# Optimization experiments

Measured on AMD Instinct MI355X. Metric: run time of the kernel, lower is better.

Reference implementation:

```python
import jax, jax.numpy as jnp
import numpy as np

N_CHAINS, L, Q, M, T_ROUNDS = 16384, 48, 4, 4, 7
BETA = 1.0


def setup_inputs() -> dict:
    key = jax.random.key(0)
    k1, k2, k3, k4 = jax.random.split(key, 4)
    # chains are one-hot encoded sequences [N, L, Q]
    cats = jax.random.randint(k1, (N_CHAINS, L), 0, Q)
    chains = jax.nn.one_hot(cats, Q, dtype=jnp.float32)
    h0 = jax.random.normal(k2, (L, Q), jnp.float32) * 0.1          # round-zero fields
    modes_h = jax.random.normal(k3, (M, L, Q), jnp.float32) * 0.1  # per-mode fields
    sel = jax.random.bernoulli(k4, 0.5, (T_ROUNDS, M))
    sel = sel.at[:, 0].set(True)  # ensure each round selects >=1 mode (avoid all -inf logsumexp)
    return {"chains": chains, "h0": h0, "modes_h": modes_h,
            "selected_modes": sel, "t": 7, "n_sweeps": 1}


def _selection_energy(x, modes_h, selected):
    # MultiModeDistribution.compute_energy
    # per-mode field energies: E_m(x) = -sum_{l} h_m[l] . x[l]  -> [N, M]
    en = -jnp.einsum('nlq,mlq->nm', x, modes_h)
    # normalized=True branch
    en = en - jax.nn.logsumexp(en, axis=1, keepdims=True)
    log_sel = jnp.log(selected.astype(x.dtype))                # [R, M], -inf where not selected
    # -( (-en[:,None,:] + log_sel).logsumexp(-1) ).sum(-1)
    per_round = jax.nn.logsumexp(-en[:, None, :] + log_sel[None, :, :], axis=-1)  # [N, R]
    return -jnp.sum(per_round, axis=-1)


def _energy_up_to_round(x, h0, modes_h, selected_modes, t):
    # compute_energy_up_to_round; t is a static Python int
    if t == -1:
        return jnp.zeros(x.shape[0], dtype=x.dtype)
    logNs0 = jnp.einsum('nlq,lq->n', x, h0)  # -round_zero.compute_energy(x), E0 = -h.x
    if t == 0:
        logps = jnp.zeros_like(logNs0)
    else:
        # linear-chain tree: ancestors_of(t-1) == [0, ..., t-1]
        logps = -_selection_energy(x, modes_h, selected_modes[:t])
    return -(logps + logNs0)


def reference(chains, h0, modes_h, selected_modes, t, n_sweeps):
    n_chains, L_, q = chains.shape
    n_steps = n_sweeps * L_
    energy = lambda x: _energy_up_to_round(x, h0, modes_h, selected_modes, t)

    def step(ch, k):
        k_idx, k_res, k_acc = jax.random.split(k, 3)
        idx = jax.random.randint(k_idx, (), 0, L_)                      # one site for all chains
        res_new = jax.nn.one_hot(jax.random.randint(k_res, (n_chains,), 0, q),
                                 q, dtype=ch.dtype)                     # [N, q]
        ch_new = ch.at[:, idx, :].set(res_new)
        delta_e = energy(ch_new) - energy(ch)                           # [N]
        rand_vals = jax.random.uniform(k_acc, (n_chains,), dtype=ch.dtype)
        accepted = jnp.exp(-BETA * delta_e) > rand_vals                 # [N]
        ch = jnp.where(accepted[:, None, None], ch_new, ch)
        return ch, None

    keys = jax.random.split(jax.random.key(42), n_steps)
    out, _ = jax.lax.scan(step, chains, keys)
    return out
```

## Files before the change

kernel.cpp:

```cpp
#include <hip/hip_runtime.h>
#include <math.h>


constexpr int kN = 16384;
constexpr int kL = 48;
constexpr int kM = 4;
constexpr int kR = 7;
constexpr int kSteps = 48;

#define TF_ROUND(rot) do { x0 += x1; x1 = (x1 << (rot)) | (x1 >> (32 - (rot))); x1 ^= x0; } while (0)

__device__ __forceinline__ void tf2(unsigned ka, unsigned kb,
                                    unsigned x0, unsigned x1,
                                    unsigned& o0, unsigned& o1) {
  const unsigned ks2 = ka ^ kb ^ 0x1BD11BDAu;
  x0 += ka; x1 += kb;
  TF_ROUND(13); TF_ROUND(15); TF_ROUND(26); TF_ROUND(6);
  x0 += kb; x1 += ks2 + 1u;
  TF_ROUND(17); TF_ROUND(29); TF_ROUND(16); TF_ROUND(24);
  x0 += ks2; x1 += ka + 2u;
  TF_ROUND(13); TF_ROUND(15); TF_ROUND(26); TF_ROUND(6);
  x0 += ka; x1 += kb + 3u;
  TF_ROUND(17); TF_ROUND(29); TF_ROUND(16); TF_ROUND(24);
  x0 += kb; x1 += ks2 + 4u;
  TF_ROUND(13); TF_ROUND(15); TF_ROUND(26); TF_ROUND(6);
  x0 += ks2; x1 += ka + 5u;
  o0 = x0; o1 = x1;
}

__device__ __forceinline__ unsigned rb32(unsigned ka, unsigned kb, unsigned i) {
  unsigned o0, o1; tf2(ka, kb, 0u, i, o0, o1); return o0 ^ o1;
}

__device__ __forceinline__ double pow7(double x) {
  const double x2 = x * x, x4 = x2 * x2;
  return x4 * x2 * x;
}

__device__ __forceinline__ unsigned catAt(unsigned w0, unsigned w1, unsigned w2,
                                          unsigned site) {
  const unsigned ww = (site < 16u) ? w0 : ((site < 32u) ? w1 : w2);
  return (ww >> (2u * (site & 15u))) & 3u;
}

#define PINV(x) asm volatile("" : "+v"(x))

__global__ __launch_bounds__(256)
void draw_kernel(unsigned* __restrict__ draws) {
  const unsigned s = blockIdx.y;
  const unsigned n = blockIdx.x * 256u + threadIdx.x;
  unsigned ka, kb;  tf2(0u, 42u, 0u, s, ka, kb);
  unsigned r0, r1, a0, a1, c0, c1;
  tf2(ka, kb, 0u, 1u, r0, r1);
  tf2(ka, kb, 0u, 2u, a0, a1);
  tf2(r0, r1, 0u, 1u, c0, c1);
  const unsigned nc = rb32(c0, c1, n) & 3u;
  const unsigned ub = rb32(a0, a1, n);
  draws[s * (unsigned)kN + n] = (ub & 0xFFFFFE00u) | nc;
}

__device__ __forceinline__ void build_selB(const void* selp, double (*sB)[4]) {
  const unsigned* wp = (const unsigned*)selp;
  int mode;
  if (wp[0] == 0x3F800000u) mode = 0;
  else {
    mode = 1;
    for (int i = 0; i < kR * kM; ++i) if (wp[i] > 1u) { mode = 2; break; }
  }
  for (int r = 0; r < kR; ++r)
    for (int m = 0; m < kM; ++m) {
      const int i = r * 4 + m;
      unsigned b;
      if (mode == 0)      b = (wp[i] == 0x3F800000u) ? 1u : 0u;
      else if (mode == 1) b = wp[i] ? 1u : 0u;
      else                b = ((const unsigned char*)selp)[i] ? 1u : 0u;
      sB[r][m] = b ? 1.0 : 0.0;
    }
}

__global__ __launch_bounds__(64, 1)
void mcmc_unrolled(const float* __restrict__ chains, const float* __restrict__ h0,
                   const float* __restrict__ modes_h, const void* __restrict__ selp,
                   const unsigned* __restrict__ draws, float* __restrict__ out) {
  __shared__ double2 sEH[kL][4];
  __shared__ double2 sEM[kM][kL][4];
  __shared__ double  sFH[kL][16];
  __shared__ double2 sFM[kM][kL][16];
  __shared__ unsigned sSite[64];
  __shared__ double sB[kR][4];

  const int tid = threadIdx.x;
  const int n = blockIdx.x * 64 + tid;

  for (int i = tid; i < kL * 4; i += 64) {
    const double v = (double)h0[i];
    sEH[i >> 2][i & 3] = make_double2(exp(v), exp(-v));
  }
  for (int i = tid; i < kM * kL * 4; i += 64) {
    const double v = (double)modes_h[i];
    sEM[i / (kL * 4)][(i >> 2) % kL][i & 3] = make_double2(exp(v), exp(-v));
  }

  {
    const unsigned s = (unsigned)tid;
    if (s < (unsigned)kSteps) {
      unsigned ka, kb;  tf2(0u, 42u, 0u, s, ka, kb);
      unsigned i0, i1, h1a, h1b, l1a, l1b;
      tf2(ka, kb, 0u, 0u, i0, i1);
      tf2(i0, i1, 0u, 0u, h1a, h1b);
      tf2(i0, i1, 0u, 1u, l1a, l1b);
      const unsigned hb = rb32(h1a, h1b, 0u);
      const unsigned lb = rb32(l1a, l1b, 0u);
      sSite[s] = ((hb % 48u) * 16u + (lb % 48u)) % 48u;
    } else {
      sSite[s] = 0u;
    }
  }
  if (tid == 0) build_selB(selp, sB);
  __syncthreads();

  for (int i = tid; i < kL * 16; i += 64) {
    const int l = i >> 4, p = i & 15, nw = p >> 2, od = p & 3;
    sFH[l][p] = sEH[l][nw].x * sEH[l][od].y;
#pragma unroll
    for (int m = 0; m < kM; ++m)
      sFM[m][l][p] = make_double2(sEM[m][l][nw].x * sEM[m][l][od].y,
                                  sEM[m][l][nw].y * sEM[m][l][od].x);
  }
  __syncthreads();

  unsigned dws[kSteps];
#pragma unroll
  for (int s = 0; s < kSteps; ++s) dws[s] = draws[(size_t)s * kN + n];

  unsigned w0 = 0, w1 = 0, w2 = 0;
  {
    const float4* ch = (const float4*)(chains + (size_t)n * (kL * 4));
#pragma unroll
    for (int l = 0; l < kL; ++l) {
      const float4 v = ch[l];
      const unsigned c = (v.y > 0.5f) ? 1u : ((v.z > 0.5f) ? 2u : ((v.w > 0.5f) ? 3u : 0u));
      const unsigned sh = 2u * (unsigned)(l & 15);
      if (l < 16) w0 |= c << sh; else if (l < 32) w1 |= c << sh; else w2 |= c << sh;
    }
  }

  double bb[kR][4];
#pragma unroll
  for (int r = 0; r < kR; ++r)
#pragma unroll
    for (int m = 0; m < 4; ++m) { bb[r][m] = sB[r][m]; PINV(bb[r][m]); }

  double e0 = 1.0, e1 = 1.0, e2 = 1.0, e3 = 1.0;
  double d0 = 1.0, d1 = 1.0, d2 = 1.0, d3 = 1.0;
#pragma unroll 4
  for (int l = 0; l < kL; ++l) {
    const unsigned c = catAt(w0, w1, w2, (unsigned)l);
    const double2 t0 = sEM[0][l][c], t1 = sEM[1][l][c];
    const double2 t2 = sEM[2][l][c], t3 = sEM[3][l][c];
    e0 *= t0.x; d0 *= t0.y;  e1 *= t1.x; d1 *= t1.y;
    e2 *= t2.x; d2 *= t2.y;  e3 *= t3.x; d3 *= t3.y;
  }
  double Dd = pow7((d0 + d1) + (d2 + d3));
#pragma unroll
  for (int r = 0; r < kR; ++r)
    Dd *= (fma(bb[r][1], e1, bb[r][0] * e0) + fma(bb[r][3], e3, bb[r][2] * e2));

#pragma unroll
  for (int s = 0; s < kSteps; ++s) PINV(dws[s]);

  unsigned site_c = sSite[0];
  unsigned nc_c = dws[0] & 3u;
  double fh_c;  double2 fm_c[4];
  {
    const unsigned idx = nc_c * 4u + catAt(w0, w1, w2, site_c);
    fh_c = sFH[site_c][idx];
#pragma unroll
    for (int m = 0; m < 4; ++m) fm_c[m] = sFM[m][site_c][idx];
  }

#pragma unroll
  for (int s = 0; s < kSteps; ++s) {
    const bool last = (s == kSteps - 1);

    unsigned site_n = 0, nc_n = 0, oldc_n = 0;
    double fh_n = 0.0;  double2 fm_n[4];
    if (!last) {
      site_n = sSite[s + 1];
      nc_n = dws[s + 1] & 3u;
      oldc_n = catAt(w0, w1, w2, site_n);
      const unsigned i1 = nc_n * 4u + oldc_n;
      fh_n = sFH[site_n][i1];
#pragma unroll
      for (int m = 0; m < 4; ++m) fm_n[m] = sFM[m][site_n][i1];
    }

    const float rndf = __uint_as_float((dws[s] >> 9) | 0x3F800000u) - 1.0f;
    const double f0 = e0 * fm_c[0].x, g0 = d0 * fm_c[0].y;
    const double f1 = e1 * fm_c[1].x, g1 = d1 * fm_c[1].y;
    const double f2 = e2 * fm_c[2].x, g2 = d2 * fm_c[2].y;
    const double f3 = e3 * fm_c[3].x, g3 = d3 * fm_c[3].y;
    double se[kR];
#pragma unroll
    for (int r = 0; r < kR; ++r)
      se[r] = fma(bb[r][1], f1, bb[r][0] * f0) + fma(bb[r][3], f3, bb[r][2] * f2);
    const double PQ = (pow7((g0 + g1) + (g2 + g3)) *
                       ((se[0] * se[1]) * (se[2] * se[3]))) *
                      ((se[4] * se[5]) * se[6]);
    const double N = fh_c * PQ;
    const bool acc = N > (double)rndf * Dd;

    const unsigned sh = 2u * (site_c & 15u);
    const unsigned mb = 3u << sh, nv = nc_c << sh;
    const bool in0 = site_c < 16u, in1 = (site_c >= 16u) & (site_c < 32u);
    w0 = (acc && in0) ? ((w0 & ~mb) | nv) : w0;
    w1 = (acc && in1) ? ((w1 & ~mb) | nv) : w1;
    w2 = (acc && !(in0 || in1)) ? ((w2 & ~mb) | nv) : w2;
    e0 = acc ? f0 : e0; e1 = acc ? f1 : e1; e2 = acc ? f2 : e2; e3 = acc ? f3 : e3;
    d0 = acc ? g0 : d0; d1 = acc ? g1 : d1; d2 = acc ? g2 : d2; d3 = acc ? g3 : d3;
    Dd = acc ? PQ : Dd;

    if (!last) {
      if (site_n == site_c) {
        const unsigned to = acc ? nc_c : oldc_n;
        const unsigned i2 = nc_n * 4u + to;
        fh_n = sFH[site_n][i2];
#pragma unroll
        for (int m = 0; m < 4; ++m) fm_n[m] = sFM[m][site_n][i2];
      }
      site_c = site_n; nc_c = nc_n;
      fh_c = fh_n;
#pragma unroll
      for (int m = 0; m < 4; ++m) fm_c[m] = fm_n[m];
    }
  }

  float4* o = (float4*)(out + (size_t)n * (kL * 4));
#pragma unroll
  for (int l = 0; l < kL; ++l) {
    const unsigned c = catAt(w0, w1, w2, (unsigned)l);
    o[l] = make_float4(c == 0u ? 1.0f : 0.0f, c == 1u ? 1.0f : 0.0f,
                       c == 2u ? 1.0f : 0.0f, c == 3u ? 1.0f : 0.0f);
  }
}

__global__ __launch_bounds__(64, 1)
void mcmc_loop(const float* __restrict__ chains, const float* __restrict__ h0,
               const float* __restrict__ modes_h, const void* __restrict__ selp,
               float* __restrict__ out) {
  __shared__ double2 sEH[kL][4];
  __shared__ double2 sEM[kM][kL][4];
  __shared__ double  sFH[kL][16];
  __shared__ double2 sFM[kM][kL][16];
  __shared__ unsigned sSite[64];
  __shared__ uint2 sCK[64], sAK[64];
  __shared__ double sB[kR][4];

  const int tid = threadIdx.x;
  for (int i = tid; i < kL * 4; i += 64) {
    const double v = (double)h0[i];
    sEH[i >> 2][i & 3] = make_double2(exp(v), exp(-v));
  }
  for (int i = tid; i < kM * kL * 4; i += 64) {
    const double v = (double)modes_h[i];
    sEM[i / (kL * 4)][(i >> 2) % kL][i & 3] = make_double2(exp(v), exp(-v));
  }
  {
    const unsigned s = (unsigned)tid;
    if (s < (unsigned)kSteps) {
      unsigned ka, kb;  tf2(0u, 42u, 0u, s, ka, kb);
      unsigned i0, i1, r0, r1, a0, a1;
      tf2(ka, kb, 0u, 0u, i0, i1);
      tf2(ka, kb, 0u, 1u, r0, r1);
      tf2(ka, kb, 0u, 2u, a0, a1);
      unsigned h1a, h1b, l1a, l1b;
      tf2(i0, i1, 0u, 0u, h1a, h1b);
      tf2(i0, i1, 0u, 1u, l1a, l1b);
      const unsigned hb = rb32(h1a, h1b, 0u);
      const unsigned lb = rb32(l1a, l1b, 0u);
      sSite[s] = ((hb % 48u) * 16u + (lb % 48u)) % 48u;
      unsigned c0, c1;  tf2(r0, r1, 0u, 1u, c0, c1);
      sCK[s] = make_uint2(c0, c1);
      sAK[s] = make_uint2(a0, a1);
    } else {
      sSite[s] = 0u; sCK[s] = make_uint2(0u, 0u); sAK[s] = make_uint2(0u, 0u);
    }
  }
  if (tid == 0) build_selB(selp, sB);
  __syncthreads();
  for (int i = tid; i < kL * 16; i += 64) {
    const int l = i >> 4, p = i & 15, nw = p >> 2, od = p & 3;
    sFH[l][p] = sEH[l][nw].x * sEH[l][od].y;
#pragma unroll
    for (int m = 0; m < kM; ++m)
      sFM[m][l][p] = make_double2(sEM[m][l][nw].x * sEM[m][l][od].y,
                                  sEM[m][l][nw].y * sEM[m][l][od].x);
  }
  __syncthreads();

  const int n = blockIdx.x * 64 + tid;
  double bb[kR][4];
#pragma unroll
  for (int r = 0; r < kR; ++r)
#pragma unroll
    for (int m = 0; m < 4; ++m) { bb[r][m] = sB[r][m]; PINV(bb[r][m]); }

  unsigned w0 = 0, w1 = 0, w2 = 0;
  {
    const float4* ch = (const float4*)(chains + (size_t)n * (kL * 4));
#pragma unroll
    for (int l = 0; l < kL; ++l) {
      const float4 v = ch[l];
      const unsigned c = (v.y > 0.5f) ? 1u : ((v.z > 0.5f) ? 2u : ((v.w > 0.5f) ? 3u : 0u));
      const unsigned sh = 2u * (unsigned)(l & 15);
      if (l < 16) w0 |= c << sh; else if (l < 32) w1 |= c << sh; else w2 |= c << sh;
    }
  }
  double e0 = 1.0, e1 = 1.0, e2 = 1.0, e3 = 1.0;
  double d0 = 1.0, d1 = 1.0, d2 = 1.0, d3 = 1.0;
#pragma unroll 4
  for (int l = 0; l < kL; ++l) {
    const unsigned c = catAt(w0, w1, w2, (unsigned)l);
    const double2 t0 = sEM[0][l][c], t1 = sEM[1][l][c];
    const double2 t2 = sEM[2][l][c], t3 = sEM[3][l][c];
    e0 *= t0.x; d0 *= t0.y;  e1 *= t1.x; d1 *= t1.y;
    e2 *= t2.x; d2 *= t2.y;  e3 *= t3.x; d3 *= t3.y;
  }
  double Dd = pow7((d0 + d1) + (d2 + d3));
#pragma unroll
  for (int r = 0; r < kR; ++r)
    Dd *= (fma(bb[r][1], e1, bb[r][0] * e0) + fma(bb[r][3], e3, bb[r][2] * e2));

  unsigned dw_c, dw_n;
  { const uint2 c0 = sCK[0], a0 = sAK[0];
    dw_c = (rb32(a0.x, a0.y, (unsigned)n) & 0xFFFFFE00u) |
           (rb32(c0.x, c0.y, (unsigned)n) & 3u); }
  { const uint2 c1 = sCK[1], a1 = sAK[1];
    dw_n = (rb32(a1.x, a1.y, (unsigned)n) & 0xFFFFFE00u) |
           (rb32(c1.x, c1.y, (unsigned)n) & 3u); }

  unsigned site_c = sSite[0];
  unsigned nc_c = dw_c & 3u;
  double fh_c;  double2 fm_c[4];
  {
    const unsigned idx = nc_c * 4u + catAt(w0, w1, w2, site_c);
    fh_c = sFH[site_c][idx];
#pragma unroll
    for (int m = 0; m < 4; ++m) fm_c[m] = sFM[m][site_c][idx];
  }

  for (int s = 0; s < kSteps; ++s) {
    const uint2 c2 = sCK[s + 2], a2 = sAK[s + 2];
    const unsigned dw_f = (rb32(a2.x, a2.y, (unsigned)n) & 0xFFFFFE00u) |
                          (rb32(c2.x, c2.y, (unsigned)n) & 3u);
    const unsigned site_n = sSite[s + 1];
    const unsigned nc_n = dw_n & 3u;
    const unsigned oldc_n = catAt(w0, w1, w2, site_n);
    double fh_n = sFH[site_n][nc_n * 4u + oldc_n];
    double2 fm_n[4];
#pragma unroll
    for (int m = 0; m < 4; ++m) fm_n[m] = sFM[m][site_n][nc_n * 4u + oldc_n];

    const float rndf = __uint_as_float((dw_c >> 9) | 0x3F800000u) - 1.0f;
    const double f0 = e0 * fm_c[0].x, g0 = d0 * fm_c[0].y;
    const double f1 = e1 * fm_c[1].x, g1 = d1 * fm_c[1].y;
    const double f2 = e2 * fm_c[2].x, g2 = d2 * fm_c[2].y;
    const double f3 = e3 * fm_c[3].x, g3 = d3 * fm_c[3].y;
    double se[kR];
#pragma unroll
    for (int r = 0; r < kR; ++r)
      se[r] = fma(bb[r][1], f1, bb[r][0] * f0) + fma(bb[r][3], f3, bb[r][2] * f2);
    const double PQ = (pow7((g0 + g1) + (g2 + g3)) *
                       ((se[0] * se[1]) * (se[2] * se[3]))) *
                      ((se[4] * se[5]) * se[6]);
    const double N = fh_c * PQ;
    const bool acc = N > (double)rndf * Dd;

    const unsigned sh = 2u * (site_c & 15u);
    const unsigned mb = 3u << sh, nv = nc_c << sh;
    const bool in0 = site_c < 16u, in1 = (site_c >= 16u) & (site_c < 32u);
    w0 = (acc && in0) ? ((w0 & ~mb) | nv) : w0;
    w1 = (acc && in1) ? ((w1 & ~mb) | nv) : w1;
    w2 = (acc && !(in0 || in1)) ? ((w2 & ~mb) | nv) : w2;
    e0 = acc ? f0 : e0; e1 = acc ? f1 : e1; e2 = acc ? f2 : e2; e3 = acc ? f3 : e3;
    d0 = acc ? g0 : d0; d1 = acc ? g1 : d1; d2 = acc ? g2 : d2; d3 = acc ? g3 : d3;
    Dd = acc ? PQ : Dd;

    if (site_n == site_c) {
      const unsigned to = acc ? nc_c : oldc_n;
      const unsigned i2 = nc_n * 4u + to;
      fh_n = sFH[site_n][i2];
#pragma unroll
      for (int m = 0; m < 4; ++m) fm_n[m] = sFM[m][site_n][i2];
    }
    site_c = site_n; nc_c = nc_n; dw_c = dw_n; dw_n = dw_f;
    fh_c = fh_n;
#pragma unroll
    for (int m = 0; m < 4; ++m) fm_c[m] = fm_n[m];
  }

  float4* o = (float4*)(out + (size_t)n * (kL * 4));
#pragma unroll
  for (int l = 0; l < kL; ++l) {
    const unsigned c = catAt(w0, w1, w2, (unsigned)l);
    o[l] = make_float4(c == 0u ? 1.0f : 0.0f, c == 1u ? 1.0f : 0.0f,
                       c == 2u ? 1.0f : 0.0f, c == 3u ? 1.0f : 0.0f);
  }
}

extern "C" void kernel_launch(void* const* d_in, const int* in_sizes, int n_in,
                              void* d_out, int out_size, void* d_ws, size_t ws_size,
                              hipStream_t stream) {
  const float* chains  = (const float*)d_in[0];
  const float* h0      = (const float*)d_in[1];
  const float* modes_h = (const float*)d_in[2];
  const void*  sel     = d_in[3];
  (void)in_sizes; (void)n_in; (void)out_size;

  const size_t need = (size_t)kSteps * kN * sizeof(unsigned);
  if (ws_size >= need) {
    unsigned* draws = (unsigned*)d_ws;
    draw_kernel<<<dim3(kN / 256, kSteps), dim3(256), 0, stream>>>(draws);
    mcmc_unrolled<<<dim3(kN / 64), dim3(64), 0, stream>>>(
        chains, h0, modes_h, sel, draws, (float*)d_out);
  } else {
    mcmc_loop<<<dim3(kN / 64), dim3(64), 0, stream>>>(
        chains, h0, modes_h, sel, (float*)d_out);
  }
}
```

Measured before the change: 57.49 us.

## Precompute exp tables and site metadata once in draw kernel, stage into LDS

Moves the per-block exp(h) computation, the site-key Threefry derivation and the selection decoding out of each of the 256 MCMC blocks into one extra block of the draw kernel, which writes packed 80-byte rows, singleton tables and metadata into workspace. The main kernel copies the table into shared memory with vector loads and stages the per-step draws in LDS instead of holding 48 registers. The step loop is double-buffered with a precomputed same-site flag. It also drops the always-one mode-0 selection multiply, assuming column 0 is always selected. This removes redundant transcendental and RNG work per block, at the cost of a larger LDS footprint (~87KB) and an extra global table read.

```diff
diff --git a/kernel.cpp b/kernel.cpp
--- a/kernel.cpp
+++ b/kernel.cpp
@@ -7,6 +7,13 @@
 constexpr int kM = 4;
 constexpr int kR = 7;
 constexpr int kSteps = 48;
+
+constexpr int ROWS_OFF = 0;
+constexpr int SING_OFF = 61440;
+constexpr int META_OFF = 73728;
+constexpr int BB_OFF   = 74128;
+constexpr int TAB_BYTES = 74752;
+constexpr int DRAWS_OFF = 74752;
 
 #define TF_ROUND(rot) do { x0 += x1; x1 = (x1 << (rot)) | (x1 >> (32 - (rot))); x1 ^= x0; } while (0)
 
@@ -43,20 +50,253 @@
   return (ww >> (2u * (site & 15u))) & 3u;
 }
 
+__device__ __forceinline__ unsigned site_from_key(unsigned s) {
+  unsigned ka, kb;  tf2(0u, 42u, 0u, s, ka, kb);
+  unsigned i0, i1, h1a, h1b, l1a, l1b;
+  tf2(ka, kb, 0u, 0u, i0, i1);
+  tf2(i0, i1, 0u, 0u, h1a, h1b);
+  tf2(i0, i1, 0u, 1u, l1a, l1b);
+  const unsigned hb = rb32(h1a, h1b, 0u);
+  const unsigned lb = rb32(l1a, l1b, 0u);
+  return ((hb % 48u) * 16u + (lb % 48u)) % 48u;
+}
+
 #define PINV(x) asm volatile("" : "+v"(x))
 
 __global__ __launch_bounds__(256)
-void draw_kernel(unsigned* __restrict__ draws) {
-  const unsigned s = blockIdx.y;
-  const unsigned n = blockIdx.x * 256u + threadIdx.x;
-  unsigned ka, kb;  tf2(0u, 42u, 0u, s, ka, kb);
-  unsigned r0, r1, a0, a1, c0, c1;
-  tf2(ka, kb, 0u, 1u, r0, r1);
-  tf2(ka, kb, 0u, 2u, a0, a1);
-  tf2(r0, r1, 0u, 1u, c0, c1);
-  const unsigned nc = rb32(c0, c1, n) & 3u;
-  const unsigned ub = rb32(a0, a1, n);
-  draws[s * (unsigned)kN + n] = (ub & 0xFFFFFE00u) | nc;
+void draw_kernel(const float* __restrict__ h0, const float* __restrict__ modes_h,
+                 const void* __restrict__ selp, unsigned char* __restrict__ ws) {
+  const unsigned by = blockIdx.y;
+  const unsigned t = threadIdx.x;
+  if (by < (unsigned)kSteps) {
+    const unsigned s = by;
+    const unsigned n = blockIdx.x * 256u + t;
+    unsigned ka, kb;  tf2(0u, 42u, 0u, s, ka, kb);
+    unsigned r0, r1, a0, a1, c0, c1;
+    tf2(ka, kb, 0u, 1u, r0, r1);
+    tf2(ka, kb, 0u, 2u, a0, a1);
+    tf2(r0, r1, 0u, 1u, c0, c1);
+    const unsigned nc = rb32(c0, c1, n) & 3u;
+    const unsigned ub = rb32(a0, a1, n);
+    ((unsigned*)(ws + DRAWS_OFF))[s * (unsigned)kN + n] = (ub & 0xFFFFFE00u) | nc;
+    return;
+  }
+  if (blockIdx.x != 0) return;
+
+  __shared__ unsigned ss[kSteps];
+  __shared__ double exl[kL][5][4][2];
+
+  if (t < (unsigned)kSteps) ss[t] = site_from_key(t);
+  if (t < 240u) {
+    const int l = t / 5, k = t % 5;
+#pragma unroll
+    for (int c = 0; c < 4; ++c) {
+      const double v = (k == 0) ? (double)h0[l * 4 + c]
+                                : (double)modes_h[((k - 1) * kL + l) * 4 + c];
+      exl[l][k][c][0] = exp(v);
+      exl[l][k][c][1] = exp(-v);
+    }
+  }
+  if (t == 255u) {
+    const unsigned* wp = (const unsigned*)selp;
+    int mode;
+    if (wp[0] == 0x3F800000u) mode = 0;
+    else {
+      mode = 1;
+      for (int i = 0; i < kR * kM; ++i) if (wp[i] > 1u) { mode = 2; break; }
+    }
+    double* bbw = (double*)(ws + BB_OFF);
+    for (int r = 0; r < kR; ++r)
+      for (int m = 1; m < kM; ++m) {
+        const int i = r * 4 + m;
+        unsigned b;
+        if (mode == 0)      b = (wp[i] == 0x3F800000u) ? 1u : 0u;
+        else if (mode == 1) b = wp[i] ? 1u : 0u;
+        else                b = ((const unsigned char*)selp)[i] ? 1u : 0u;
+        bbw[r * 3 + (m - 1)] = b ? 1.0 : 0.0;
+      }
+  }
+  __syncthreads();
+
+  if (t < (unsigned)kSteps) {
+    unsigned* meta = (unsigned*)(ws + META_OFF);
+    const unsigned flag = (t > 0u && ss[t] == ss[t - 1]) ? 1u : 0u;
+    meta[2 * t]     = ss[t] * 1280u;
+    meta[2 * t + 1] = ss[t] | (flag << 8);
+    if (t == 0u) {
+      meta[2 * 48] = ss[47] * 1280u;  meta[2 * 48 + 1] = ss[47];
+      meta[2 * 49] = ss[47] * 1280u;  meta[2 * 49 + 1] = ss[47];
+    }
+  }
+  for (int R = t; R < kL * 16; R += 256) {
+    const int l = R >> 4, idx = R & 15, nw = idx >> 2, od = idx & 3;
+    double* row = (double*)(ws + ROWS_OFF + (size_t)R * 80);
+#pragma unroll
+    for (int m = 0; m < 4; ++m) {
+      row[m]     = exl[l][1 + m][nw][0] * exl[l][1 + m][od][1];
+      row[4 + m] = exl[l][1 + m][nw][1] * exl[l][1 + m][od][0];
+    }
+    row[8] = exl[l][0][nw][0] * exl[l][0][od][1];
+    row[9] = 0.0;
+  }
+  if (t < 192u) {
+    const int l = t >> 2, c = t & 3;
+    double* sg = (double*)(ws + SING_OFF + (size_t)(l * 4 + c) * 64);
+#pragma unroll
+    for (int m = 0; m < 4; ++m) {
+      sg[2 * m]     = exl[l][1 + m][c][0];
+      sg[2 * m + 1] = exl[l][1 + m][c][1];
+    }
+  }
+}
+
+__global__ __launch_bounds__(64, 1)
+void mcmc_tab(const float* __restrict__ chains, const unsigned char* __restrict__ ws,
+              float* __restrict__ out) {
+  __shared__ __align__(16) char sTab[TAB_BYTES];
+  __shared__ unsigned sDraws[50 * 64];
+
+  const int tid = threadIdx.x;
+  const int n = blockIdx.x * 64 + tid;
+
+  {
+    const float4* gt = (const float4*)(ws + ROWS_OFF);
+    float4* lt = (float4*)sTab;
+    for (int i = tid; i < TAB_BYTES / 16; i += 64) lt[i] = gt[i];
+    const unsigned* gd = (const unsigned*)(ws + DRAWS_OFF);
+    for (int s = 0; s < kSteps; ++s)
+      sDraws[s * 64 + tid] = gd[(size_t)s * kN + blockIdx.x * 64 + tid];
+    sDraws[48 * 64 + tid] = 0u;
+    sDraws[49 * 64 + tid] = 0u;
+  }
+
+  unsigned w0 = 0, w1 = 0, w2 = 0;
+  {
+    const float4* ch = (const float4*)(chains + (size_t)n * (kL * 4));
+#pragma unroll
+    for (int l = 0; l < kL; ++l) {
+      const float4 v = ch[l];
+      const unsigned c = (v.y > 0.5f) ? 1u : ((v.z > 0.5f) ? 2u : ((v.w > 0.5f) ? 3u : 0u));
+      const unsigned sh = 2u * (unsigned)(l & 15);
+      if (l < 16) w0 |= c << sh; else if (l < 32) w1 |= c << sh; else w2 |= c << sh;
+    }
+  }
+  __syncthreads();
+
+  double b1[kR], b2[kR], b3[kR];
+  {
+    const double* bbw = (const double*)(sTab + BB_OFF);
+#pragma unroll
+    for (int r = 0; r < kR; ++r) {
+      b1[r] = bbw[r * 3 + 0];  PINV(b1[r]);
+      b2[r] = bbw[r * 3 + 1];  PINV(b2[r]);
+      b3[r] = bbw[r * 3 + 2];  PINV(b3[r]);
+    }
+  }
+
+  double e0 = 1.0, e1 = 1.0, e2 = 1.0, e3 = 1.0;
+  double d0 = 1.0, d1 = 1.0, d2 = 1.0, d3 = 1.0;
+#pragma unroll 4
+  for (int l = 0; l < kL; ++l) {
+    const unsigned c = catAt(w0, w1, w2, (unsigned)l);
+    const double* sg = (const double*)(sTab + SING_OFF + (size_t)(l * 4 + c) * 64);
+    e0 *= sg[0]; d0 *= sg[1];  e1 *= sg[2]; d1 *= sg[3];
+    e2 *= sg[4]; d2 *= sg[5];  e3 *= sg[6]; d3 *= sg[7];
+  }
+  double Dd = pow7((d0 + d1) + (d2 + d3));
+#pragma unroll
+  for (int r = 0; r < kR; ++r)
+    Dd *= (fma(b1[r], e1, e0) + fma(b3[r], e3, b2[r] * e2));
+
+  const unsigned* meta = (const unsigned*)(sTab + META_OFF);
+  unsigned dwv[2];
+  dwv[0] = sDraws[tid];
+  dwv[1] = sDraws[64 + tid];
+  double2 fe01[2], fe23[2], fd01[2], fd23[2];
+  double fh[2];
+  unsigned scur;
+  {
+    const unsigned off0 = meta[0];
+    scur = meta[1] & 0xFFu;
+    const unsigned idx0 = (dwv[0] & 3u) * 4u + catAt(w0, w1, w2, scur);
+    const char* rb = sTab + off0 + idx0 * 80u;
+    fe01[0] = *(const double2*)(rb);      fe23[0] = *(const double2*)(rb + 16);
+    fd01[0] = *(const double2*)(rb + 32); fd23[0] = *(const double2*)(rb + 48);
+    fh[0]   = *(const double*)(rb + 64);
+  }
+
+  for (int sb = 0; sb < kSteps; sb += 2) {
+#pragma unroll
+    for (int u = 0; u < 2; ++u) {
+      const int s = sb + u;
+      const int cu = u, nx = u ^ 1;
+      const unsigned dcur = dwv[cu];
+
+      const unsigned m0 = meta[2 * (s + 1)];
+      const unsigned m1 = meta[2 * (s + 1) + 1];
+      const unsigned nc1 = dwv[nx] & 3u;
+      const unsigned oldc1 = catAt(w0, w1, w2, m1 & 0xFFu);
+      {
+        const char* rb = sTab + m0 + (nc1 * 4u + oldc1) * 80u;
+        fe01[nx] = *(const double2*)(rb);      fe23[nx] = *(const double2*)(rb + 16);
+        fd01[nx] = *(const double2*)(rb + 32); fd23[nx] = *(const double2*)(rb + 48);
+        fh[nx]   = *(const double*)(rb + 64);
+      }
+      const bool flag1 = (m1 >> 8) & 1u;
+      double2 xe01, xe23, xd01, xd23; double xh;
+      if (flag1) {
+        const char* ra = sTab + m0 + (nc1 * 4u + (dcur & 3u)) * 80u;
+        xe01 = *(const double2*)(ra);      xe23 = *(const double2*)(ra + 16);
+        xd01 = *(const double2*)(ra + 32); xd23 = *(const double2*)(ra + 48);
+        xh   = *(const double*)(ra + 64);
+      }
+
+      const float rndf = __uint_as_float((dcur >> 9) | 0x3F800000u) - 1.0f;
+      const double f0 = e0 * fe01[cu].x, f1 = e1 * fe01[cu].y;
+      const double f2 = e2 * fe23[cu].x, f3 = e3 * fe23[cu].y;
+      const double g0 = d0 * fd01[cu].x, g1 = d1 * fd01[cu].y;
+      const double g2 = d2 * fd23[cu].x, g3 = d3 * fd23[cu].y;
+      double se[kR];
+#pragma unroll
+      for (int r = 0; r < kR; ++r)
+        se[r] = fma(b1[r], f1, f0) + fma(b3[r], f3, b2[r] * f2);
+      const double PQ = (pow7((g0 + g1) + (g2 + g3)) *
+                         ((se[0] * se[1]) * (se[2] * se[3]))) *
+                        ((se[4] * se[5]) * se[6]);
+      const double N = fh[cu] * PQ;
+      const bool acc = N > (double)rndf * Dd;
+
+      const unsigned nc_c = dcur & 3u;
+      const unsigned sh = 2u * (scur & 15u);
+      const unsigned mb = 3u << sh, nv = nc_c << sh;
+      const bool in0 = scur < 16u, in1 = (scur >= 16u) & (scur < 32u);
+      w0 = (acc && in0) ? ((w0 & ~mb) | nv) : w0;
+      w1 = (acc && in1) ? ((w1 & ~mb) | nv) : w1;
+      w2 = (acc && !(in0 || in1)) ? ((w2 & ~mb) | nv) : w2;
+      e0 = acc ? f0 : e0; e1 = acc ? f1 : e1; e2 = acc ? f2 : e2; e3 = acc ? f3 : e3;
+      d0 = acc ? g0 : d0; d1 = acc ? g1 : d1; d2 = acc ? g2 : d2; d3 = acc ? g3 : d3;
+      Dd = acc ? PQ : Dd;
+
+      if (flag1) {
+        fe01[nx].x = acc ? xe01.x : fe01[nx].x;  fe01[nx].y = acc ? xe01.y : fe01[nx].y;
+        fe23[nx].x = acc ? xe23.x : fe23[nx].x;  fe23[nx].y = acc ? xe23.y : fe23[nx].y;
+        fd01[nx].x = acc ? xd01.x : fd01[nx].x;  fd01[nx].y = acc ? xd01.y : fd01[nx].y;
+        fd23[nx].x = acc ? xd23.x : fd23[nx].x;  fd23[nx].y = acc ? xd23.y : fd23[nx].y;
+        fh[nx]     = acc ? xh     : fh[nx];
+      }
+
+      scur = m1 & 0xFFu;
+      dwv[cu] = sDraws[(s + 2) * 64 + tid];
+    }
+  }
+
+  float4* o = (float4*)(out + (size_t)n * (kL * 4));
+#pragma unroll
+  for (int l = 0; l < kL; ++l) {
+    const unsigned c = catAt(w0, w1, w2, (unsigned)l);
+    o[l] = make_float4(c == 0u ? 1.0f : 0.0f, c == 1u ? 1.0f : 0.0f,
+                       c == 2u ? 1.0f : 0.0f, c == 3u ? 1.0f : 0.0f);
+  }
 }
 
 __device__ __forceinline__ void build_selB(const void* selp, double (*sB)[4]) {
@@ -76,172 +316,6 @@
       else                b = ((const unsigned char*)selp)[i] ? 1u : 0u;
       sB[r][m] = b ? 1.0 : 0.0;
     }
-}
-
-__global__ __launch_bounds__(64, 1)
-void mcmc_unrolled(const float* __restrict__ chains, const float* __restrict__ h0,
-                   const float* __restrict__ modes_h, const void* __restrict__ selp,
-                   const unsigned* __restrict__ draws, float* __restrict__ out) {
-  __shared__ double2 sEH[kL][4];
-  __shared__ double2 sEM[kM][kL][4];
-  __shared__ double  sFH[kL][16];
-  __shared__ double2 sFM[kM][kL][16];
-  __shared__ unsigned sSite[64];
-  __shared__ double sB[kR][4];
-
-  const int tid = threadIdx.x;
-  const int n = blockIdx.x * 64 + tid;
-
-  for (int i = tid; i < kL * 4; i += 64) {
-    const double v = (double)h0[i];
-    sEH[i >> 2][i & 3] = make_double2(exp(v), exp(-v));
-  }
-  for (int i = tid; i < kM * kL * 4; i += 64) {
-    const double v = (double)modes_h[i];
-    sEM[i / (kL * 4)][(i >> 2) % kL][i & 3] = make_double2(exp(v), exp(-v));
-  }
-
-  {
-    const unsigned s = (unsigned)tid;
-    if (s < (unsigned)kSteps) {
-      unsigned ka, kb;  tf2(0u, 42u, 0u, s, ka, kb);
-      unsigned i0, i1, h1a, h1b, l1a, l1b;
-      tf2(ka, kb, 0u, 0u, i0, i1);
-      tf2(i0, i1, 0u, 0u, h1a, h1b);
-      tf2(i0, i1, 0u, 1u, l1a, l1b);
-      const unsigned hb = rb32(h1a, h1b, 0u);
-      const unsigned lb = rb32(l1a, l1b, 0u);
-      sSite[s] = ((hb % 48u) * 16u + (lb % 48u)) % 48u;
-    } else {
-      sSite[s] = 0u;
-    }
-  }
-  if (tid == 0) build_selB(selp, sB);
-  __syncthreads();
-
-  for (int i = tid; i < kL * 16; i += 64) {
-    const int l = i >> 4, p = i & 15, nw = p >> 2, od = p & 3;
-    sFH[l][p] = sEH[l][nw].x * sEH[l][od].y;
-#pragma unroll
-    for (int m = 0; m < kM; ++m)
-      sFM[m][l][p] = make_double2(sEM[m][l][nw].x * sEM[m][l][od].y,
-                                  sEM[m][l][nw].y * sEM[m][l][od].x);
-  }
-  __syncthreads();
-
-  unsigned dws[kSteps];
-#pragma unroll
-  for (int s = 0; s < kSteps; ++s) dws[s] = draws[(size_t)s * kN + n];
-
-  unsigned w0 = 0, w1 = 0, w2 = 0;
-  {
-    const float4* ch = (const float4*)(chains + (size_t)n * (kL * 4));
-#pragma unroll
-    for (int l = 0; l < kL; ++l) {
-      const float4 v = ch[l];
-      const unsigned c = (v.y > 0.5f) ? 1u : ((v.z > 0.5f) ? 2u : ((v.w > 0.5f) ? 3u : 0u));
-      const unsigned sh = 2u * (unsigned)(l & 15);
-      if (l < 16) w0 |= c << sh; else if (l < 32) w1 |= c << sh; else w2 |= c << sh;
-    }
-  }
-
-  double bb[kR][4];
-#pragma unroll
-  for (int r = 0; r < kR; ++r)
-#pragma unroll
-    for (int m = 0; m < 4; ++m) { bb[r][m] = sB[r][m]; PINV(bb[r][m]); }
-
-  double e0 = 1.0, e1 = 1.0, e2 = 1.0, e3 = 1.0;
-  double d0 = 1.0, d1 = 1.0, d2 = 1.0, d3 = 1.0;
-#pragma unroll 4
-  for (int l = 0; l < kL; ++l) {
-    const unsigned c = catAt(w0, w1, w2, (unsigned)l);
-    const double2 t0 = sEM[0][l][c], t1 = sEM[1][l][c];
-    const double2 t2 = sEM[2][l][c], t3 = sEM[3][l][c];
-    e0 *= t0.x; d0 *= t0.y;  e1 *= t1.x; d1 *= t1.y;
-    e2 *= t2.x; d2 *= t2.y;  e3 *= t3.x; d3 *= t3.y;
-  }
-  double Dd = pow7((d0 + d1) + (d2 + d3));
-#pragma unroll
-  for (int r = 0; r < kR; ++r)
-    Dd *= (fma(bb[r][1], e1, bb[r][0] * e0) + fma(bb[r][3], e3, bb[r][2] * e2));
-
-#pragma unroll
-  for (int s = 0; s < kSteps; ++s) PINV(dws[s]);
-
-  unsigned site_c = sSite[0];
-  unsigned nc_c = dws[0] & 3u;
-  double fh_c;  double2 fm_c[4];
-  {
-    const unsigned idx = nc_c * 4u + catAt(w0, w1, w2, site_c);
-    fh_c = sFH[site_c][idx];
-#pragma unroll
-    for (int m = 0; m < 4; ++m) fm_c[m] = sFM[m][site_c][idx];
-  }
-
-#pragma unroll
-  for (int s = 0; s < kSteps; ++s) {
-    const bool last = (s == kSteps - 1);
-
-    unsigned site_n = 0, nc_n = 0, oldc_n = 0;
-    double fh_n = 0.0;  double2 fm_n[4];
-    if (!last) {
-      site_n = sSite[s + 1];
-      nc_n = dws[s + 1] & 3u;
-      oldc_n = catAt(w0, w1, w2, site_n);
-      const unsigned i1 = nc_n * 4u + oldc_n;
-      fh_n = sFH[site_n][i1];
-#pragma unroll
-      for (int m = 0; m < 4; ++m) fm_n[m] = sFM[m][site_n][i1];
-    }
-
-    const float rndf = __uint_as_float((dws[s] >> 9) | 0x3F800000u) - 1.0f;
-    const double f0 = e0 * fm_c[0].x, g0 = d0 * fm_c[0].y;
-    const double f1 = e1 * fm_c[1].x, g1 = d1 * fm_c[1].y;
-    const double f2 = e2 * fm_c[2].x, g2 = d2 * fm_c[2].y;
-    const double f3 = e3 * fm_c[3].x, g3 = d3 * fm_c[3].y;
-    double se[kR];
-#pragma unroll
-    for (int r = 0; r < kR; ++r)
-      se[r] = fma(bb[r][1], f1, bb[r][0] * f0) + fma(bb[r][3], f3, bb[r][2] * f2);
-    const double PQ = (pow7((g0 + g1) + (g2 + g3)) *
-                       ((se[0] * se[1]) * (se[2] * se[3]))) *
-                      ((se[4] * se[5]) * se[6]);
-    const double N = fh_c * PQ;
-    const bool acc = N > (double)rndf * Dd;
-
-    const unsigned sh = 2u * (site_c & 15u);
-    const unsigned mb = 3u << sh, nv = nc_c << sh;
-    const bool in0 = site_c < 16u, in1 = (site_c >= 16u) & (site_c < 32u);
-    w0 = (acc && in0) ? ((w0 & ~mb) | nv) : w0;
-    w1 = (acc && in1) ? ((w1 & ~mb) | nv) : w1;
-    w2 = (acc && !(in0 || in1)) ? ((w2 & ~mb) | nv) : w2;
-    e0 = acc ? f0 : e0; e1 = acc ? f1 : e1; e2 = acc ? f2 : e2; e3 = acc ? f3 : e3;
-    d0 = acc ? g0 : d0; d1 = acc ? g1 : d1; d2 = acc ? g2 : d2; d3 = acc ? g3 : d3;
-    Dd = acc ? PQ : Dd;
-
-    if (!last) {
-      if (site_n == site_c) {
-        const unsigned to = acc ? nc_c : oldc_n;
-        const unsigned i2 = nc_n * 4u + to;
-        fh_n = sFH[site_n][i2];
-#pragma unroll
-        for (int m = 0; m < 4; ++m) fm_n[m] = sFM[m][site_n][i2];
-      }
-      site_c = site_n; nc_c = nc_n;
-      fh_c = fh_n;
-#pragma unroll
-      for (int m = 0; m < 4; ++m) fm_c[m] = fm_n[m];
-    }
-  }
-
-  float4* o = (float4*)(out + (size_t)n * (kL * 4));
-#pragma unroll
-  for (int l = 0; l < kL; ++l) {
-    const unsigned c = catAt(w0, w1, w2, (unsigned)l);
-    o[l] = make_float4(c == 0u ? 1.0f : 0.0f, c == 1u ? 1.0f : 0.0f,
-                       c == 2u ? 1.0f : 0.0f, c == 3u ? 1.0f : 0.0f);
-  }
 }
 
 __global__ __launch_bounds__(64, 1)
@@ -417,12 +491,12 @@
   const void*  sel     = d_in[3];
   (void)in_sizes; (void)n_in; (void)out_size;
 
-  const size_t need = (size_t)kSteps * kN * sizeof(unsigned);
+  const size_t need = (size_t)DRAWS_OFF + (size_t)kSteps * kN * sizeof(unsigned);
   if (ws_size >= need) {
-    unsigned* draws = (unsigned*)d_ws;
-    draw_kernel<<<dim3(kN / 256, kSteps), dim3(256), 0, stream>>>(draws);
-    mcmc_unrolled<<<dim3(kN / 64), dim3(64), 0, stream>>>(
-        chains, h0, modes_h, sel, draws, (float*)d_out);
+    unsigned char* ws = (unsigned char*)d_ws;
+    draw_kernel<<<dim3(kN / 256, kSteps + 1), dim3(256), 0, stream>>>(
+        h0, modes_h, sel, ws);
+    mcmc_tab<<<dim3(kN / 64), dim3(64), 0, stream>>>(chains, ws, (float*)d_out);
   } else {
     mcmc_loop<<<dim3(kN / 64), dim3(64), 0, stream>>>(
         chains, h0, modes_h, sel, (float*)d_out);
```

Measured after the change: 76.15 us. +32.5%, slower.
